# Kernel tuning notes

Measured on AMD Instinct MI355X. Metric: run time of the kernel, lower is better.

The kernel has to match this reference:

```python
import jax, jax.numpy as jnp
import numpy as np

H = 12       # num attention heads
D = 64       # head dim
K = 6        # heads activated: max(1, int(H * top_k_percent)), top_k_percent=0.5
EPS = 1e-12  # BERT LayerNorm eps


def setup_inputs() -> dict:
    key = jax.random.key(0)
    ks = jax.random.split(key, 8)
    hid = H * D
    sc = 0.02
    return {
        'hidden_states': jax.random.normal(ks[0], (8, 1024, hid), jnp.float32),
        'Wq': jax.random.normal(ks[1], (hid, hid), jnp.float32) * sc,
        'bq': jnp.zeros((hid,), jnp.float32),
        'Wk': jax.random.normal(ks[2], (hid, hid), jnp.float32) * sc,
        'bk': jnp.zeros((hid,), jnp.float32),
        'Wv': jax.random.normal(ks[3], (hid, hid), jnp.float32) * sc,
        'bv': jnp.zeros((hid,), jnp.float32),
        'Wr': jax.random.normal(ks[4], (hid, H), jnp.float32) * sc,
        'br': jnp.zeros((H,), jnp.float32),
        'Wo': jax.random.normal(ks[5], (hid, hid), jnp.float32) * sc,
        'bo': jnp.zeros((hid,), jnp.float32),
        'ln_g': jnp.ones((hid,), jnp.float32),
        'ln_b': jnp.zeros((hid,), jnp.float32),
    }


def reference(hidden_states, Wq, bq, Wk, bk, Wv, bv, Wr, br, Wo, bo, ln_g, ln_b):
    B, S, hid = hidden_states.shape
    # Router: mean-pooled tokens -> per-head logits -> straight-through top-k mask
    router_in = hidden_states.mean(axis=1)                      # [B, hid]
    logits = router_in @ Wr + br                                # [B, H]
    _, top_idx = jax.lax.top_k(logits, K)                       # [B, K]
    hard = jax.nn.one_hot(top_idx, H, dtype=logits.dtype).sum(axis=1)  # [B, H]
    head_mask = hard + logits - jax.lax.stop_gradient(logits)   # straight-through
    m = head_mask[:, :, None, None]                             # [B, H, 1, 1]

    def proj(W, b):
        return (hidden_states @ W + b).reshape(B, S, H, D).transpose(0, 2, 1, 3)

    q = proj(Wq, bq) * m
    k = proj(Wk, bk) * m
    v = proj(Wv, bv) * m

    scores = jnp.einsum('bhqd,bhkd->bhqk', q, k) / jnp.sqrt(jnp.float32(D))
    probs = jax.nn.softmax(scores, axis=-1)
    ctx = jnp.einsum('bhqk,bhkd->bhqd', probs, v)               # [B, H, S, D]
    ctx = ctx.transpose(0, 2, 1, 3).reshape(B, S, hid)

    # BertSelfOutput: dense -> (dropout=identity in eval) -> residual -> LayerNorm
    x = ctx @ Wo + bo + hidden_states
    mu = x.mean(axis=-1, keepdims=True)
    var = ((x - mu) ** 2).mean(axis=-1, keepdims=True)
    return ((x - mu) / jnp.sqrt(var + EPS)) * ln_g + ln_b
```

## Files before the change

kernel.cpp:

```cpp
#include <hip/hip_runtime.h>

typedef __bf16 bf16;
typedef __bf16 bf16x2_t __attribute__((ext_vector_type(2)));
typedef __bf16 bf16x4_t __attribute__((ext_vector_type(4)));
typedef __bf16 bf16x8 __attribute__((ext_vector_type(8)));
typedef float  f32x4  __attribute__((ext_vector_type(4)));

__device__ __forceinline__ void async16(const void* g, void* l) {
  __builtin_amdgcn_global_load_lds(
      (__attribute__((address_space(1))) void*)(g),
      (__attribute__((address_space(3))) void*)(l), 16, 0, 0);
}

__device__ __forceinline__ f32x4 mfma16(bf16x8 a, bf16x8 b, f32x4 c) {
  return __builtin_amdgcn_mfma_f32_16x16x32_bf16(a, b, c, 0, 0, 0);
}

__global__ __launch_bounds__(192) void cvt_router_k(const float* __restrict__ hs,
                                                    bf16* __restrict__ hsb,
                                                    float* __restrict__ partial) {
  int b = blockIdx.x, g = blockIdx.y, t = threadIdx.x;
  const float* p = hs  + ((size_t)b * 1024 + g * 32) * 768 + t * 4;
  bf16*        q = hsb + ((size_t)b * 1024 + g * 32) * 768 + t * 4;
  float4 a = {0.f, 0.f, 0.f, 0.f};
  for (int s = 0; s < 32; ++s) {
    float4 v = *(const float4*)(p + (size_t)s * 768);
    a.x += v.x; a.y += v.y; a.z += v.z; a.w += v.w;
    bf16x4_t o;
    o[0] = (bf16)v.x; o[1] = (bf16)v.y; o[2] = (bf16)v.z; o[3] = (bf16)v.w;
    *(bf16x4_t*)(q + (size_t)s * 768) = o;
  }
  *(float4*)(partial + ((size_t)b * 32 + g) * 768 + t * 4) = a;
}

__global__ __launch_bounds__(256) void transpose4_k(
    const float* __restrict__ s0, const float* __restrict__ s1,
    const float* __restrict__ s2, const float* __restrict__ s3,
    bf16* __restrict__ d0, bf16* __restrict__ d1,
    bf16* __restrict__ d2, bf16* __restrict__ d3) {
  __shared__ bf16 tile[32][33];
  int z = blockIdx.z;
  const float* in = (z == 0) ? s0 : (z == 1) ? s1 : (z == 2) ? s2 : s3;
  bf16* out       = (z == 0) ? d0 : (z == 1) ? d1 : (z == 2) ? d2 : d3;
  int c0 = blockIdx.x * 32, r0 = blockIdx.y * 32;
  int t = threadIdx.x;
#pragma unroll
  for (int i = 0; i < 4; ++i) {
    int idx = t + i * 256;
    int r = idx >> 5, c = idx & 31;
    tile[r][c] = (bf16)in[(size_t)(r0 + r) * 768 + (c0 + c)];
  }
  __syncthreads();
#pragma unroll
  for (int i = 0; i < 4; ++i) {
    int idx = t + i * 256;
    int r = idx >> 5, c = idx & 31;
    out[(size_t)(c0 + r) * 768 + (r0 + c)] = tile[c][r];
  }
}

__global__ __launch_bounds__(256) void router_final_k(const float* __restrict__ Wr,
                                                      const float* __restrict__ br,
                                                      const float* __restrict__ partial,
                                                      float* __restrict__ mask,
                                                      int* __restrict__ actH) {
  int b = blockIdx.x, t = threadIdx.x;
  int w = t >> 6;
  __shared__ float mean_s[768];
  __shared__ float red[4][12];
  __shared__ float lg[12];
  for (int c = t; c < 768; c += 256) {
    float a = 0.f;
    for (int g = 0; g < 32; ++g) a += partial[((size_t)b * 32 + g) * 768 + c];
    mean_s[c] = a * (1.0f / 1024.0f);
  }
  __syncthreads();
  float a[12];
#pragma unroll
  for (int h = 0; h < 12; ++h) a[h] = 0.f;
#pragma unroll
  for (int j = 0; j < 3; ++j) {
    int c = t + j * 256;
    float m = mean_s[c];
    const float* wr = Wr + c * 12;
#pragma unroll
    for (int h = 0; h < 12; ++h) a[h] += m * wr[h];
  }
#pragma unroll
  for (int off = 1; off < 64; off <<= 1)
#pragma unroll
    for (int h = 0; h < 12; ++h) a[h] += __shfl_xor(a[h], off);
  if ((t & 63) == 0)
#pragma unroll
    for (int h = 0; h < 12; ++h) red[w][h] = a[h];
  __syncthreads();
  if (t == 0) {
#pragma unroll
    for (int h = 0; h < 12; ++h)
      lg[h] = br[h] + red[0][h] + red[1][h] + red[2][h] + red[3][h];
    unsigned chosen = 0;
    for (int j = 0; j < 6; ++j) {
      int bi = -1; float bv = -1e30f;
      for (int h = 0; h < 12; ++h)
        if (!((chosen >> h) & 1) && lg[h] > bv) { bv = lg[h]; bi = h; }
      chosen |= 1u << bi;
    }
    int k = 0;
    for (int h = 0; h < 12; ++h) {
      mask[b * 12 + h] = ((chosen >> h) & 1) ? 1.f : 0.f;
      if ((chosen >> h) & 1) actH[b * 6 + (k++)] = h;
    }
  }
}

__global__ __launch_bounds__(256, 3) void gemm_qkv_k(
    const bf16* __restrict__ X, const bf16* __restrict__ Wcat,
    const float* __restrict__ bq, const float* __restrict__ bk, const float* __restrict__ bv,
    const int* __restrict__ actH,
    bf16* __restrict__ Qo, bf16* __restrict__ Ko, bf16* __restrict__ Vto) {
  __shared__ __align__(16) bf16 Al[128 * 64];
  __shared__ __align__(16) bf16 Bl[128 * 64];
  int mt64 = blockIdx.x;
  int sp   = blockIdx.y;
  int z    = blockIdx.z;
  int b    = mt64 >> 3;
  int h0   = actH[b * 6 + sp * 2];
  int h1   = actH[b * 6 + sp * 2 + 1];
  int m0   = mt64 * 128;

  const float* bia = (z == 0) ? bq : (z == 1) ? bk : bv;
  int t = threadIdx.x, w = t >> 6, lane = t & 63, lrow = lane & 15, quad = lane >> 4;
  int wm = (w >> 1) * 64, wn = (w & 1) * 64;

  int srow = t >> 3;
  int sch  = (t & 7) ^ (srow & 7);
  const bf16* aptr[4];
  const bf16* bptr[4];
#pragma unroll
  for (int i = 0; i < 4; ++i) {
    aptr[i] = X + (size_t)(m0 + i * 32 + srow) * 768 + sch * 8;
    int hh = (i < 2) ? h0 : h1;
    int rr = (i & 1) * 32 + srow;
    bptr[i] = Wcat + (size_t)(z * 768 + hh * 64 + rr) * 768 + sch * 8;
  }

  int ra_base = wm + lrow, rb_base = wn + lrow;
  const bf16* baA[2];
  const bf16* baB[2];
#pragma unroll
  for (int ks = 0; ks < 2; ++ks) {
    baA[ks] = &Al[ra_base * 64 + (((ks * 4 + quad) ^ (ra_base & 7)) * 8)];
    baB[ks] = &Bl[rb_base * 64 + (((ks * 4 + quad) ^ (rb_base & 7)) * 8)];
  }

  f32x4 acc[4][4];
#pragma unroll
  for (int a = 0; a < 4; ++a)
#pragma unroll
    for (int c = 0; c < 4; ++c) acc[a][c] = (f32x4){0.f, 0.f, 0.f, 0.f};

  for (int k0 = 0; k0 < 768; k0 += 64) {
#pragma unroll
    for (int i = 0; i < 4; ++i) {
      async16(aptr[i], &Al[(i * 256 + t) * 8]);
      aptr[i] += 64;
    }
#pragma unroll
    for (int i = 0; i < 4; ++i) {
      async16(bptr[i], &Bl[(i * 256 + t) * 8]);
      bptr[i] += 64;
    }
    __syncthreads();
    bf16x8 af[2][4], bfr[2][4];
#pragma unroll
    for (int ks = 0; ks < 2; ++ks)
#pragma unroll
      for (int i = 0; i < 4; ++i) {
        af[ks][i]  = *(const bf16x8*)(baA[ks] + i * 1024);
        bfr[ks][i] = *(const bf16x8*)(baB[ks] + i * 1024);
      }
#pragma unroll
    for (int ks = 0; ks < 2; ++ks)
#pragma unroll
      for (int mt = 0; mt < 4; ++mt)
#pragma unroll
        for (int nt2 = 0; nt2 < 4; ++nt2)
          acc[mt][nt2] = mfma16(af[ks][mt], bfr[ks][nt2], acc[mt][nt2]);
    __syncthreads();
  }

  float biasv[4];
#pragma unroll
  for (int nt2 = 0; nt2 < 4; ++nt2) {
    int nl = wn + nt2 * 16 + lrow;
    int hh = (nl >> 6) ? h1 : h0;
    biasv[nt2] = bia[hh * 64 + (nl & 63)];
  }

  if (z == 2) {
#pragma unroll
    for (int mt = 0; mt < 4; ++mt)
#pragma unroll
      for (int nt2 = 0; nt2 < 4; ++nt2) {
        int s = (m0 + wm + mt * 16 + quad * 4) & 1023;
        int nl = wn + nt2 * 16 + lrow;
        int hh = (nl >> 6) ? h1 : h0;
        int d = nl & 63;
        bf16x4_t pk;
#pragma unroll
        for (int r = 0; r < 4; ++r) pk[r] = (bf16)(acc[mt][nt2][r] + biasv[nt2]);
        *(bf16x4_t*)&Vto[(((size_t)b * 12 + hh) * 64 + d) * 1024 + s] = pk;
      }
  } else {
    bf16* Out = (z == 0) ? Qo : Ko;
#pragma unroll
    for (int mt = 0; mt < 4; ++mt)
#pragma unroll
      for (int nt2 = 0; nt2 < 4; ++nt2)
#pragma unroll
        for (int r = 0; r < 4; ++r) {
          int s = (m0 + wm + mt * 16 + quad * 4 + r) & 1023;
          int nl = wn + nt2 * 16 + lrow;
          int hh = (nl >> 6) ? h1 : h0;
          int d = nl & 63;
          Out[(((size_t)b * 12 + hh) * 1024 + s) * 64 + d] =
              (bf16)(acc[mt][nt2][r] + biasv[nt2]);
        }
  }
}

__global__ __launch_bounds__(256, 3) void attn_k(
    const bf16* __restrict__ Q, const bf16* __restrict__ K, const bf16* __restrict__ Vt,
    const int* __restrict__ actH, bf16* __restrict__ ctx) {
  int ai = blockIdx.x, qt = blockIdx.y;
  int bb = ai / 6, slot = ai - bb * 6;
  int h = actH[bb * 6 + slot];
  int bh = bb * 12 + h;
  int t = threadIdx.x, w = t >> 6, lane = t & 63, lrow = lane & 15, quad = lane >> 4;

  __shared__ __align__(16) bf16 K_lds[128 * 64];
  __shared__ __align__(16) bf16 V_lds[64 * 128];
  __shared__ __align__(16) bf16 P_lds[4][16 * 136];

  const bf16* Qh = Q  + (size_t)bh * 65536;
  const bf16* Kh = K  + (size_t)bh * 65536;
  const bf16* Vh = Vt + (size_t)bh * 65536;

  bf16x8 qf[2][2];
#pragma unroll
  for (int mt = 0; mt < 2; ++mt)
#pragma unroll
    for (int ks = 0; ks < 2; ++ks)
      qf[mt][ks] = *(const bf16x8*)&Qh[(size_t)(qt * 128 + w * 32 + mt * 16 + lrow) * 64 + ks * 32 + quad * 8];

  f32x4 o_acc[2][4];
  float m_i[2][4], l_i[2][4];
#pragma unroll
  for (int mt = 0; mt < 2; ++mt) {
#pragma unroll
    for (int dt = 0; dt < 4; ++dt) o_acc[mt][dt] = (f32x4){0.f, 0.f, 0.f, 0.f};
#pragma unroll
    for (int r = 0; r < 4; ++r) { m_i[mt][r] = -INFINITY; l_i[mt][r] = 0.f; }
  }

  for (int kt = 0; kt < 8; ++kt) {
#pragma unroll
    for (int i = 0; i < 4; ++i) {
      int c = i * 256 + t;
      int r = c >> 3, ch = (c & 7) ^ (r & 7);
      async16(Kh + (size_t)kt * 8192 + r * 64 + ch * 8, &K_lds[c * 8]);
    }
#pragma unroll
    for (int i = 0; i < 4; ++i) {
      int c = i * 256 + t;
      int r = c >> 4, ch = (c & 15) ^ (r & 7);
      async16(Vh + (size_t)r * 1024 + kt * 128 + ch * 8, &V_lds[c * 8]);
    }
    __syncthreads();

#pragma unroll
    for (int mt = 0; mt < 2; ++mt) {
      f32x4 s_acc[8];
#pragma unroll
      for (int nt = 0; nt < 8; ++nt) s_acc[nt] = (f32x4){0.f, 0.f, 0.f, 0.f};
#pragma unroll
      for (int nt = 0; nt < 8; ++nt) {
        int rb = nt * 16 + lrow;
#pragma unroll
        for (int ks = 0; ks < 2; ++ks) {
          bf16x8 kf = *(const bf16x8*)&K_lds[rb * 64 + (((ks * 4 + quad) ^ (rb & 7)) * 8)];
          s_acc[nt] = mfma16(qf[mt][ks], kf, s_acc[nt]);
        }
      }
#pragma unroll
      for (int nt = 0; nt < 8; ++nt) s_acc[nt] = s_acc[nt] * 0.125f;

#pragma unroll
      for (int r = 0; r < 4; ++r) {
        float mx = s_acc[0][r];
#pragma unroll
        for (int nt = 1; nt < 8; ++nt) mx = fmaxf(mx, s_acc[nt][r]);
        mx = fmaxf(mx, __shfl_xor(mx, 1));
        mx = fmaxf(mx, __shfl_xor(mx, 2));
        mx = fmaxf(mx, __shfl_xor(mx, 4));
        mx = fmaxf(mx, __shfl_xor(mx, 8));
        float mold = m_i[mt][r];
        float mnew = fmaxf(mold, mx);
        float alpha = __expf(mold - mnew);
        m_i[mt][r] = mnew;
        float rs = 0.f;
#pragma unroll
        for (int nt = 0; nt < 8; ++nt) {
          float pv = __expf(s_acc[nt][r] - mnew);
          rs += pv;
          P_lds[w][(quad * 4 + r) * 136 + nt * 16 + lrow] = (bf16)pv;
        }
        rs += __shfl_xor(rs, 1);
        rs += __shfl_xor(rs, 2);
        rs += __shfl_xor(rs, 4);
        rs += __shfl_xor(rs, 8);
        l_i[mt][r] = l_i[mt][r] * alpha + rs;
#pragma unroll
        for (int dt = 0; dt < 4; ++dt) o_acc[mt][dt][r] *= alpha;
      }

      bf16x8 pf[4];
#pragma unroll
      for (int ks = 0; ks < 4; ++ks)
        pf[ks] = *(const bf16x8*)&P_lds[w][lrow * 136 + ks * 32 + quad * 8];
#pragma unroll
      for (int dt = 0; dt < 4; ++dt) {
        int rv = dt * 16 + lrow;
#pragma unroll
        for (int ks = 0; ks < 4; ++ks) {
          bf16x8 vf = *(const bf16x8*)&V_lds[rv * 128 + (((ks * 4 + quad) ^ (rv & 7)) * 8)];
          o_acc[mt][dt] = mfma16(pf[ks], vf, o_acc[mt][dt]);
        }
      }
    }
    __syncthreads();
  }

#pragma unroll
  for (int mt = 0; mt < 2; ++mt)
#pragma unroll
    for (int r = 0; r < 4; ++r) {
      float inv = 1.0f / l_i[mt][r];
      int s = qt * 128 + w * 32 + mt * 16 + quad * 4 + r;
#pragma unroll
      for (int dt = 0; dt < 4; ++dt) {
        int d = dt * 16 + lrow;
        ctx[((size_t)(bb * 1024 + s)) * 768 + h * 64 + d] = (bf16)(o_acc[mt][dt][r] * inv);
      }
    }
}

__global__ __launch_bounds__(256, 3) void gemm_out_k(
    const bf16* __restrict__ Cx, const bf16* __restrict__ Wot,
    const float* __restrict__ bo, const float* __restrict__ res,
    const float* __restrict__ mask,
    float* __restrict__ xo) {
  __shared__ __align__(16) bf16 Al[128 * 64];
  __shared__ __align__(16) bf16 Bl[128 * 64];
  int bid = blockIdx.x;
  int xcd = bid & 7, idx = bid >> 3;
  int nt = idx % 6, mt8 = idx / 6;
  int m0 = (mt8 * 8 + xcd) * 128;
  int n0 = nt * 128;
  int t = threadIdx.x, w = t >> 6, lane = t & 63, lrow = lane & 15, quad = lane >> 4;
  int wm = (w >> 1) * 64, wn = (w & 1) * 64;

  int bb = m0 >> 10;
  unsigned am = 0;
#pragma unroll
  for (int hh = 0; hh < 12; ++hh)
    am |= (mask[bb * 12 + hh] != 0.f) ? (1u << hh) : 0u;

  int srow = t >> 3;
  int sch  = (t & 7) ^ (srow & 7);
  const bf16* aptr[4];
  const bf16* bptr[4];
#pragma unroll
  for (int i = 0; i < 4; ++i) {
    aptr[i] = Cx  + (size_t)(m0 + i * 32 + srow) * 768 + sch * 8;
    bptr[i] = Wot + (size_t)(n0 + i * 32 + srow) * 768 + sch * 8;
  }
  int ra_base = wm + lrow, rb_base = wn + lrow;
  const bf16* baA[2];
  const bf16* baB[2];
#pragma unroll
  for (int ks = 0; ks < 2; ++ks) {
    baA[ks] = &Al[ra_base * 64 + (((ks * 4 + quad) ^ (ra_base & 7)) * 8)];
    baB[ks] = &Bl[rb_base * 64 + (((ks * 4 + quad) ^ (rb_base & 7)) * 8)];
  }

  f32x4 acc[4][4];
#pragma unroll
  for (int a = 0; a < 4; ++a)
#pragma unroll
    for (int b = 0; b < 4; ++b) acc[a][b] = (f32x4){0.f, 0.f, 0.f, 0.f};

  for (int k0 = 0; k0 < 768; k0 += 64) {
    if (am & (1u << (k0 >> 6))) {
#pragma unroll
      for (int i = 0; i < 4; ++i) async16(aptr[i], &Al[(i * 256 + t) * 8]);
#pragma unroll
      for (int i = 0; i < 4; ++i) async16(bptr[i], &Bl[(i * 256 + t) * 8]);
      __syncthreads();
      bf16x8 af[2][4], bfr[2][4];
#pragma unroll
      for (int ks = 0; ks < 2; ++ks)
#pragma unroll
        for (int i = 0; i < 4; ++i) {
          af[ks][i]  = *(const bf16x8*)(baA[ks] + i * 1024);
          bfr[ks][i] = *(const bf16x8*)(baB[ks] + i * 1024);
        }
#pragma unroll
      for (int ks = 0; ks < 2; ++ks)
#pragma unroll
        for (int mt = 0; mt < 4; ++mt)
#pragma unroll
          for (int nt2 = 0; nt2 < 4; ++nt2)
            acc[mt][nt2] = mfma16(af[ks][mt], bfr[ks][nt2], acc[mt][nt2]);
      __syncthreads();
    }
#pragma unroll
    for (int i = 0; i < 4; ++i) { aptr[i] += 64; bptr[i] += 64; }
  }

  float biasv[4];
#pragma unroll
  for (int nt2 = 0; nt2 < 4; ++nt2) biasv[nt2] = bo[n0 + wn + nt2 * 16 + lrow];

#pragma unroll
  for (int mt = 0; mt < 4; ++mt)
#pragma unroll
    for (int nt2 = 0; nt2 < 4; ++nt2)
#pragma unroll
      for (int r = 0; r < 4; ++r) {
        int m = m0 + wm + mt * 16 + quad * 4 + r;
        int n = n0 + wn + nt2 * 16 + lrow;
        xo[(size_t)m * 768 + n] = acc[mt][nt2][r] + biasv[nt2] + res[(size_t)m * 768 + n];
      }
}

__global__ __launch_bounds__(256) void ln_k(const float* __restrict__ x,
                                            const float* __restrict__ g,
                                            const float* __restrict__ be,
                                            float* __restrict__ out) {
  int row = blockIdx.x, t = threadIdx.x;
  const float* xr = x + (size_t)row * 768;
  float v0 = xr[t], v1 = xr[t + 256], v2 = xr[t + 512];
  float s = v0 + v1 + v2;
  float s2 = v0 * v0 + v1 * v1 + v2 * v2;
#pragma unroll
  for (int off = 32; off > 0; off >>= 1) {
    s  += __shfl_down(s, off);
    s2 += __shfl_down(s2, off);
  }
  __shared__ float red[8];
  if ((t & 63) == 0) { red[(t >> 6) * 2] = s; red[(t >> 6) * 2 + 1] = s2; }
  __syncthreads();
  if (t == 0) {
    float a = 0.f, b2 = 0.f;
    for (int i = 0; i < 4; ++i) { a += red[2 * i]; b2 += red[2 * i + 1]; }
    float mu = a * (1.0f / 768.0f);
    float var = b2 * (1.0f / 768.0f) - mu * mu;
    red[0] = mu;
    red[1] = rsqrtf(var + 1e-12f);
  }
  __syncthreads();
  float mu = red[0], rs = red[1];
  out[(size_t)row * 768 + t]       = (v0 - mu) * rs * g[t]       + be[t];
  out[(size_t)row * 768 + t + 256] = (v1 - mu) * rs * g[t + 256] + be[t + 256];
  out[(size_t)row * 768 + t + 512] = (v2 - mu) * rs * g[t + 512] + be[t + 512];
}

extern "C" void kernel_launch(void* const* d_in, const int* in_sizes, int n_in,
                              void* d_out, int out_size, void* d_ws, size_t ws_size,
                              hipStream_t stream) {
  const float* hs  = (const float*)d_in[0];
  const float* Wq  = (const float*)d_in[1];
  const float* bq  = (const float*)d_in[2];
  const float* Wk  = (const float*)d_in[3];
  const float* bk  = (const float*)d_in[4];
  const float* Wv  = (const float*)d_in[5];
  const float* bv  = (const float*)d_in[6];
  const float* Wr  = (const float*)d_in[7];
  const float* br  = (const float*)d_in[8];
  const float* Wo  = (const float*)d_in[9];
  const float* bo  = (const float*)d_in[10];
  const float* lng = (const float*)d_in[11];
  const float* lnb = (const float*)d_in[12];
  float* out = (float*)d_out;
  dim3 blk(256);

  char* p = (char*)d_ws;
  float* maskp = (float*)p; p += 512;
  int*   actI  = (int*)p;   p += 256;
  float* partial = (float*)p; p += (size_t)8 * 32 * 768 * 4;
  bf16* hsb  = (bf16*)p; p += (size_t)8192 * 768 * 2;
  bf16* Wcat = (bf16*)p; p += (size_t)2304 * 768 * 2;
  bf16* Wot  = (bf16*)p; p += (size_t)768 * 768 * 2;

  cvt_router_k<<<dim3(8, 32), dim3(192), 0, stream>>>(hs, hsb, partial);
  transpose4_k<<<dim3(24, 24, 4), blk, 0, stream>>>(
      Wq, Wk, Wv, Wo, Wcat, Wcat + 768 * 768, Wcat + 1536 * 768, Wot);
  router_final_k<<<dim3(8), blk, 0, stream>>>(Wr, br, partial, maskp, actI);

  size_t used_common = (size_t)(p - (char*)d_ws);
  size_t need_big = used_common + 3 * (size_t)8192 * 768 * 2;

  if (ws_size >= need_big) {
    char* qk_base = p;
    bf16* Qb  = (bf16*)p; p += (size_t)8192 * 768 * 2;
    bf16* Kb  = (bf16*)p; p += (size_t)8192 * 768 * 2;
    bf16* Vtb = (bf16*)p;
    float* Xb = (float*)qk_base;
    bf16* Ctx = (bf16*)d_out;

    gemm_qkv_k<<<dim3(64, 3, 3), blk, 0, stream>>>(hsb, Wcat, bq, bk, bv, actI, Qb, Kb, Vtb);
    attn_k<<<dim3(48, 8), blk, 0, stream>>>(Qb, Kb, Vtb, actI, Ctx);
    gemm_out_k<<<dim3(8 * 8 * 6), blk, 0, stream>>>(Ctx, Wot, bo, hs, maskp, Xb);
    ln_k<<<dim3(8192), blk, 0, stream>>>(Xb, lng, lnb, out);
  } else {
    bf16* Qb  = (bf16*)p; p += (size_t)1024 * 768 * 2;
    bf16* Kb  = (bf16*)p; p += (size_t)1024 * 768 * 2;
    bf16* Vtb = (bf16*)p; p += (size_t)1024 * 768 * 2;
    bf16* Ctx = (bf16*)p; p += (size_t)1024 * 768 * 2;
    float* Xb = (float*)p; p += (size_t)1024 * 768 * 4;

    for (int b = 0; b < 8; ++b) {
      const bf16* hsb_b = hsb + (size_t)b * 1024 * 768;
      const float* hs_b = hs + (size_t)b * 1024 * 768;
      float* outb = out + (size_t)b * 1024 * 768;
      gemm_qkv_k<<<dim3(8, 3, 3), blk, 0, stream>>>(hsb_b, Wcat, bq, bk, bv, actI + b * 6, Qb, Kb, Vtb);
      attn_k<<<dim3(6, 8), blk, 0, stream>>>(Qb, Kb, Vtb, actI + b * 6, Ctx);
      gemm_out_k<<<dim3(8 * 1 * 6), blk, 0, stream>>>(Ctx, Wot, bo, hs_b, maskp + b * 12, Xb);
      ln_k<<<dim3(1024), blk, 0, stream>>>(Xb, lng, lnb, outb);
    }
  }
}
```

Baseline: 214.3 us.

## Merge prep kernels, add lazy softmax rescale and MFMA priority hints in attention

Fuses the hidden-state conversion/router partial-sum kernel and the weight transpose kernel into one launch, which removes a kernel launch and lets the two independent jobs overlap. In the attention inner loop, the running max and the accumulator rescale are only updated when some lane's block max exceeds the stored max by more than 8 (a conditional, lazy rescale). This skips the exp and multiply work on most tiles. The MFMA sections are also wrapped with s_setprio. The lazy rescale allows exponentials up to e^8 in bf16 P values, which may cost some precision, and adds a wave-wide vote with divergence.

```diff
diff --git a/kernel.cpp b/kernel.cpp
--- a/kernel.cpp
+++ b/kernel.cpp
@@ -16,46 +16,49 @@
   return __builtin_amdgcn_mfma_f32_16x16x32_bf16(a, b, c, 0, 0, 0);
 }
 
-__global__ __launch_bounds__(192) void cvt_router_k(const float* __restrict__ hs,
-                                                    bf16* __restrict__ hsb,
-                                                    float* __restrict__ partial) {
-  int b = blockIdx.x, g = blockIdx.y, t = threadIdx.x;
-  const float* p = hs  + ((size_t)b * 1024 + g * 32) * 768 + t * 4;
-  bf16*        q = hsb + ((size_t)b * 1024 + g * 32) * 768 + t * 4;
-  float4 a = {0.f, 0.f, 0.f, 0.f};
-  for (int s = 0; s < 32; ++s) {
-    float4 v = *(const float4*)(p + (size_t)s * 768);
-    a.x += v.x; a.y += v.y; a.z += v.z; a.w += v.w;
-    bf16x4_t o;
-    o[0] = (bf16)v.x; o[1] = (bf16)v.y; o[2] = (bf16)v.z; o[3] = (bf16)v.w;
-    *(bf16x4_t*)(q + (size_t)s * 768) = o;
-  }
-  *(float4*)(partial + ((size_t)b * 32 + g) * 768 + t * 4) = a;
-}
-
-__global__ __launch_bounds__(256) void transpose4_k(
+__global__ __launch_bounds__(256) void prep_k(
+    const float* __restrict__ hs, bf16* __restrict__ hsb, float* __restrict__ partial,
     const float* __restrict__ s0, const float* __restrict__ s1,
     const float* __restrict__ s2, const float* __restrict__ s3,
     bf16* __restrict__ d0, bf16* __restrict__ d1,
     bf16* __restrict__ d2, bf16* __restrict__ d3) {
   __shared__ bf16 tile[32][33];
-  int z = blockIdx.z;
-  const float* in = (z == 0) ? s0 : (z == 1) ? s1 : (z == 2) ? s2 : s3;
-  bf16* out       = (z == 0) ? d0 : (z == 1) ? d1 : (z == 2) ? d2 : d3;
-  int c0 = blockIdx.x * 32, r0 = blockIdx.y * 32;
+  int id = blockIdx.x;
   int t = threadIdx.x;
-#pragma unroll
-  for (int i = 0; i < 4; ++i) {
-    int idx = t + i * 256;
-    int r = idx >> 5, c = idx & 31;
-    tile[r][c] = (bf16)in[(size_t)(r0 + r) * 768 + (c0 + c)];
-  }
-  __syncthreads();
-#pragma unroll
-  for (int i = 0; i < 4; ++i) {
-    int idx = t + i * 256;
-    int r = idx >> 5, c = idx & 31;
-    out[(size_t)(c0 + r) * 768 + (r0 + c)] = tile[c][r];
+  if (id < 2304) {
+    int z = id / 576, rem = id % 576;
+    int by = rem / 24, bx = rem % 24;
+    const float* in = (z == 0) ? s0 : (z == 1) ? s1 : (z == 2) ? s2 : s3;
+    bf16* out       = (z == 0) ? d0 : (z == 1) ? d1 : (z == 2) ? d2 : d3;
+    int c0 = bx * 32, r0 = by * 32;
+#pragma unroll
+    for (int i = 0; i < 4; ++i) {
+      int idx = t + i * 256;
+      int r = idx >> 5, c = idx & 31;
+      tile[r][c] = (bf16)in[(size_t)(r0 + r) * 768 + (c0 + c)];
+    }
+    __syncthreads();
+#pragma unroll
+    for (int i = 0; i < 4; ++i) {
+      int idx = t + i * 256;
+      int r = idx >> 5, c = idx & 31;
+      out[(size_t)(c0 + r) * 768 + (r0 + c)] = tile[c][r];
+    }
+  } else {
+    int id2 = id - 2304;
+    int b = id2 & 7, g = id2 >> 3;
+    if (t >= 192) return;
+    const float* p = hs  + ((size_t)b * 1024 + g * 32) * 768 + t * 4;
+    bf16*        q = hsb + ((size_t)b * 1024 + g * 32) * 768 + t * 4;
+    float4 a = {0.f, 0.f, 0.f, 0.f};
+    for (int s = 0; s < 32; ++s) {
+      float4 v = *(const float4*)(p + (size_t)s * 768);
+      a.x += v.x; a.y += v.y; a.z += v.z; a.w += v.w;
+      bf16x4_t o;
+      o[0] = (bf16)v.x; o[1] = (bf16)v.y; o[2] = (bf16)v.z; o[3] = (bf16)v.w;
+      *(bf16x4_t*)(q + (size_t)s * 768) = o;
+    }
+    *(float4*)(partial + ((size_t)b * 32 + g) * 768 + t * 4) = a;
   }
 }
 
@@ -283,6 +286,7 @@
       f32x4 s_acc[8];
 #pragma unroll
       for (int nt = 0; nt < 8; ++nt) s_acc[nt] = (f32x4){0.f, 0.f, 0.f, 0.f};
+      __builtin_amdgcn_s_setprio(1);
 #pragma unroll
       for (int nt = 0; nt < 8; ++nt) {
         int rb = nt * 16 + lrow;
@@ -292,22 +296,40 @@
           s_acc[nt] = mfma16(qf[mt][ks], kf, s_acc[nt]);
         }
       }
+      __builtin_amdgcn_s_setprio(0);
 #pragma unroll
       for (int nt = 0; nt < 8; ++nt) s_acc[nt] = s_acc[nt] * 0.125f;
 
+      float mx[4];
 #pragma unroll
       for (int r = 0; r < 4; ++r) {
-        float mx = s_acc[0][r];
-#pragma unroll
-        for (int nt = 1; nt < 8; ++nt) mx = fmaxf(mx, s_acc[nt][r]);
-        mx = fmaxf(mx, __shfl_xor(mx, 1));
-        mx = fmaxf(mx, __shfl_xor(mx, 2));
-        mx = fmaxf(mx, __shfl_xor(mx, 4));
-        mx = fmaxf(mx, __shfl_xor(mx, 8));
-        float mold = m_i[mt][r];
-        float mnew = fmaxf(mold, mx);
-        float alpha = __expf(mold - mnew);
-        m_i[mt][r] = mnew;
+        float m = s_acc[0][r];
+#pragma unroll
+        for (int nt = 1; nt < 8; ++nt) m = fmaxf(m, s_acc[nt][r]);
+        m = fmaxf(m, __shfl_xor(m, 1));
+        m = fmaxf(m, __shfl_xor(m, 2));
+        m = fmaxf(m, __shfl_xor(m, 4));
+        m = fmaxf(m, __shfl_xor(m, 8));
+        mx[r] = m;
+      }
+      bool grow = false;
+#pragma unroll
+      for (int r = 0; r < 4; ++r) grow = grow || (mx[r] > m_i[mt][r] + 8.f);
+      if (__any(grow)) {
+#pragma unroll
+        for (int r = 0; r < 4; ++r) {
+          float mold = m_i[mt][r];
+          float mnew = fmaxf(mold, mx[r]);
+          float alpha = __expf(mold - mnew);
+          m_i[mt][r] = mnew;
+          l_i[mt][r] *= alpha;
+#pragma unroll
+          for (int dt = 0; dt < 4; ++dt) o_acc[mt][dt][r] *= alpha;
+        }
+      }
+#pragma unroll
+      for (int r = 0; r < 4; ++r) {
+        float mnew = m_i[mt][r];
         float rs = 0.f;
 #pragma unroll
         for (int nt = 0; nt < 8; ++nt) {
@@ -319,15 +341,14 @@
         rs += __shfl_xor(rs, 2);
         rs += __shfl_xor(rs, 4);
         rs += __shfl_xor(rs, 8);
-        l_i[mt][r] = l_i[mt][r] * alpha + rs;
-#pragma unroll
-        for (int dt = 0; dt < 4; ++dt) o_acc[mt][dt][r] *= alpha;
+        l_i[mt][r] += rs;
       }
 
       bf16x8 pf[4];
 #pragma unroll
       for (int ks = 0; ks < 4; ++ks)
         pf[ks] = *(const bf16x8*)&P_lds[w][lrow * 136 + ks * 32 + quad * 8];
+      __builtin_amdgcn_s_setprio(1);
 #pragma unroll
       for (int dt = 0; dt < 4; ++dt) {
         int rv = dt * 16 + lrow;
@@ -337,6 +358,7 @@
           o_acc[mt][dt] = mfma16(pf[ks], vf, o_acc[mt][dt]);
         }
       }
+      __builtin_amdgcn_s_setprio(0);
     }
     __syncthreads();
   }
@@ -503,8 +525,7 @@
   bf16* Wcat = (bf16*)p; p += (size_t)2304 * 768 * 2;
   bf16* Wot  = (bf16*)p; p += (size_t)768 * 768 * 2;
 
-  cvt_router_k<<<dim3(8, 32), dim3(192), 0, stream>>>(hs, hsb, partial);
-  transpose4_k<<<dim3(24, 24, 4), blk, 0, stream>>>(
+  prep_k<<<dim3(2560), blk, 0, stream>>>(hs, hsb, partial,
       Wq, Wk, Wv, Wo, Wcat, Wcat + 768 * 768, Wcat + 1536 * 768, Wot);
   router_final_k<<<dim3(8), blk, 0, stream>>>(Wr, br, partial, maskp, actI);
 
```

Result: faster. 208.3 us (-2.8%).
